# Optimization experiments

Hardware: AMD Instinct MI355X
Metric: run time of the kernel (lower is better)

The kernel has to match this reference:

```python
import jax, jax.numpy as jnp
import numpy as np

B, P = 65536, 22  # sets, max players per freeze frame
IN, HID, OUT = 6, 64, 128


def setup_inputs() -> dict:
    key = jax.random.key(0)
    k0, k1, k2, k3, k4, k5 = jax.random.split(key, 6)
    pitch = jnp.array([120.0, 80.0], dtype=jnp.float32)
    player_locs = jax.random.uniform(k0, (B, P, 2), dtype=jnp.float32) * pitch
    actor_locs = jax.random.uniform(k1, (B, 2), dtype=jnp.float32) * pitch
    # teammate / keeper flags in {0,1}
    flags = jax.random.randint(k2, (B, P, 2), 0, 2).astype(jnp.float32)
    # validity mask: 0 -> player skipped (simulates ragged / missing entries)
    mask = jax.random.randint(k3, (B, P), 0, 2).astype(jnp.int32)
    W1 = jax.random.normal(k4, (IN, HID), dtype=jnp.float32) / np.sqrt(IN)
    b1 = jnp.zeros((HID,), dtype=jnp.float32)
    W2 = jax.random.normal(k5, (HID, OUT), dtype=jnp.float32) / np.sqrt(HID)
    b2 = jnp.zeros((OUT,), dtype=jnp.float32)
    return {"player_locs": player_locs, "actor_locs": actor_locs, "flags": flags,
            "mask": mask, "W1": W1, "b1": b1, "W2": W2, "b2": b2}


def reference(player_locs, actor_locs, flags, mask, W1, b1, W2, b2):
    # per-player features relative to the actor: [dx, dy, dist, angle, teammate, keeper]
    dxy = player_locs - actor_locs[:, None, :]                 # [B,P,2]
    dist = jnp.sqrt(jnp.sum(dxy * dxy, axis=-1, keepdims=True))  # [B,P,1]
    angle = jnp.arctan2(dxy[..., 1:2], dxy[..., 0:1])            # [B,P,1]
    feats = jnp.concatenate([dxy, dist, angle, flags], axis=-1)  # [B,P,6]
    # PlayerMLP: Linear -> ReLU -> Linear
    h = jax.nn.relu(jnp.einsum('bpi,ih->bph', feats, W1) + b1)   # [B,P,64]
    emb = jnp.einsum('bph,ho->bpo', h, W2) + b2                  # [B,P,128]
    # masked mean over valid players; empty sets yield zeros (sum is 0)
    m = mask.astype(emb.dtype)[..., None]                        # [B,P,1]
    cnt = jnp.sum(m, axis=1)                                     # [B,1]
    pooled = jnp.sum(emb * m, axis=1) / jnp.maximum(cnt, 1.0)    # [B,128]
    return pooled
```

## Files before the change

### kernel.cpp

```cpp
#include <hip/hip_runtime.h>
#include <math.h>

#define PMAX 22
#define HID 64
#define OUTD 128
#define SETS_PER_WAVE 8
#define WAVES_PER_BLOCK 4

typedef __attribute__((ext_vector_type(8))) short short8;
typedef __attribute__((ext_vector_type(4))) float float4v;

__device__ __forceinline__ float rl(float v, int l) {
    return __int_as_float(__builtin_amdgcn_readlane(__float_as_int(v), l));
}
__device__ __forceinline__ unsigned bf16_bits(float x) {
    unsigned u = __float_as_uint(x);
    return (u + 0x7FFFu + ((u >> 16) & 1u)) >> 16;
}
__device__ __forceinline__ void wave_lds_sync() {
    asm volatile("s_waitcnt lgkmcnt(0)" ::: "memory");
    __builtin_amdgcn_wave_barrier();
}

__global__ __launch_bounds__(256) void set_encoder_kernel(
    const float* __restrict__ player_locs,
    const float* __restrict__ actor_locs,
    const float* __restrict__ flags,
    const int*   __restrict__ mask,
    const float* __restrict__ W1,
    const float* __restrict__ b1,
    const float* __restrict__ W2,
    const float* __restrict__ b2,
    float* __restrict__ out)
{
    __shared__ __align__(16) unsigned w2f[16 * 256];
    __shared__ __align__(16) unsigned short hb[WAVES_PER_BLOCK][SETS_PER_WAVE][HID + 4];

    const int tid  = threadIdx.x;
    const int lane = tid & 63;
    const int wave = tid >> 6;

    const int wave_id = blockIdx.x * WAVES_PER_BLOCK + wave;
    const int set0    = wave_id * SETS_PER_WAVE;

    {
        const int pr = tid >> 3;
        const int nt = tid & 7;
        const float* rA = W2 + (size_t)(2 * pr) * OUTD + 16 * nt;
        const float* rB = rA + OUTD;
        float ra[16], rb[16];
#pragma unroll
        for (int i = 0; i < 4; ++i) {
            *(float4*)&ra[4 * i] = ((const float4*)rA)[i];
            *(float4*)&rb[4 * i] = ((const float4*)rB)[i];
        }
        const int kt = pr >> 4;
        const int kk = (2 * pr) & 31;
        const int Q  = kk >> 3;
        const int j2 = (kk >> 1) & 3;
        const int base = ((kt * 8 + nt) * 4 + Q) * 64 + j2;
#pragma unroll
        for (int c = 0; c < 16; ++c)
            w2f[base + 4 * c] = bf16_bits(ra[c]) | (bf16_bits(rb[c]) << 16);
    }

    const float w10 = W1[0 * HID + lane];
    const float w11 = W1[1 * HID + lane];
    const float w12 = W1[2 * HID + lane];
    const float w13 = W1[3 * HID + lane];
    const float w14 = W1[4 * HID + lane];
    const float w15 = W1[5 * HID + lane];
    const float b1l = b1[lane];

    __syncthreads();

    float fr[4][6];
    unsigned long long bm[4];
#pragma unroll
    for (int g = 0; g < 4; ++g) {
        const int lidx = lane < 2 * PMAX ? lane : 2 * PMAX - 1;
        const int grow = (set0 + 2 * g) * PMAX + lidx;
        float2 pl = ((const float2*)player_locs)[grow];
        float2 fl = ((const float2*)flags)[grow];
        int    m  = mask[grow];
        const int sl = 2 * g + (lidx >= PMAX ? 1 : 0);
        float2 ac = ((const float2*)actor_locs)[set0 + sl];
        float dx = pl.x - ac.x;
        float dy = pl.y - ac.y;
        fr[g][0] = dx;
        fr[g][1] = dy;
        fr[g][2] = sqrtf(dx * dx + dy * dy);
        fr[g][3] = atan2f(dy, dx);
        fr[g][4] = fl.x;
        fr[g][5] = fl.y;
        bm[g] = __ballot((lane < 2 * PMAX) && (m != 0));
    }

    float hs[SETS_PER_WAVE];
    unsigned nonempty = 0;
#pragma unroll
    for (int s = 0; s < SETS_PER_WAVE; ++s) {
        const int g    = s >> 1;
        const int base = (s & 1) * PMAX;
        unsigned bits = (unsigned)(bm[g] >> base) & 0x3FFFFFu;
        const int cnt = __builtin_popcount(bits);
        if (bits) nonempty |= (1u << s);
        float acc = 0.0f;
        unsigned bb = bits;
        while (bb) {
            const int p = __builtin_ctz(bb);
            bb &= bb - 1;
            const int src = base + p;
            float f0 = rl(fr[g][0], src);
            float f1 = rl(fr[g][1], src);
            float f2 = rl(fr[g][2], src);
            float f3 = rl(fr[g][3], src);
            float f4 = rl(fr[g][4], src);
            float f5 = rl(fr[g][5], src);
            float t0 = fmaf(f0, w10, b1l);
            t0 = fmaf(f1, w11, t0);
            t0 = fmaf(f2, w12, t0);
            float t1 = f3 * w13;
            t1 = fmaf(f4, w14, t1);
            t1 = fmaf(f5, w15, t1);
            acc += fmaxf(t0 + t1, 0.0f);
        }
        hs[s] = acc * (1.0f / fmaxf((float)cnt, 1.0f));
    }

#pragma unroll
    for (int s = 0; s < SETS_PER_WAVE; ++s)
        hb[wave][s][lane] = (unsigned short)bf16_bits(hs[s]);
    wave_lds_sync();

    const int Q  = lane >> 4;
    const int sA = lane & 7;
    short8 afrag[2];
#pragma unroll
    for (int kt = 0; kt < 2; ++kt) {
        uint2 p0 = *(const uint2*)&hb[wave][sA][32 * kt + 8 * Q];
        uint2 p1 = *(const uint2*)&hb[wave][sA][32 * kt + 8 * Q + 4];
        union { unsigned u[4]; short8 s8; } cv;
        cv.u[0] = p0.x; cv.u[1] = p0.y; cv.u[2] = p1.x; cv.u[3] = p1.y;
        afrag[kt] = cv.s8;
    }

    float4v acc[8];
#pragma unroll
    for (int nt = 0; nt < 8; ++nt) {
        union { uint4 u4; short8 s8; } f0, f1;
        f0.u4 = *(const uint4*)&w2f[(0 * 8 + nt) * 256 + 4 * lane];
        f1.u4 = *(const uint4*)&w2f[(1 * 8 + nt) * 256 + 4 * lane];
        float4v z = {0.0f, 0.0f, 0.0f, 0.0f};
        acc[nt] = __builtin_amdgcn_mfma_f32_16x16x32_bf16(afrag[0], f0.s8, z, 0, 0, 0);
        acc[nt] = __builtin_amdgcn_mfma_f32_16x16x32_bf16(afrag[1], f1.s8, acc[nt], 0, 0, 0);
    }

    const int c = lane & 15;
    float b2v[8];
#pragma unroll
    for (int nt = 0; nt < 8; ++nt) b2v[nt] = b2[16 * nt + c];

    if (Q < 2) {
        const unsigned nsh = nonempty >> (4 * Q);
#pragma unroll
        for (int nt = 0; nt < 8; ++nt) {
#pragma unroll
            for (int r = 0; r < 4; ++r) {
                const int s = 4 * Q + r;
                const float f = (float)((nsh >> r) & 1u);
                out[(size_t)(set0 + s) * OUTD + 16 * nt + c] = acc[nt][r] + f * b2v[nt];
            }
        }
    }
}

extern "C" void kernel_launch(void* const* d_in, const int* in_sizes, int n_in,
                              void* d_out, int out_size, void* d_ws, size_t ws_size,
                              hipStream_t stream) {
    const float* player_locs = (const float*)d_in[0];
    const float* actor_locs  = (const float*)d_in[1];
    const float* flags       = (const float*)d_in[2];
    const int*   mask        = (const int*)d_in[3];
    const float* W1          = (const float*)d_in[4];
    const float* b1          = (const float*)d_in[5];
    const float* W2          = (const float*)d_in[6];
    const float* b2          = (const float*)d_in[7];
    float*       out         = (float*)d_out;

    const int B = in_sizes[0] / (PMAX * 2);
    const int sets_per_block = WAVES_PER_BLOCK * SETS_PER_WAVE;
    const int grid = (B + sets_per_block - 1) / sets_per_block;

    hipLaunchKernelGGL(set_encoder_kernel, dim3(grid), dim3(256), 0, stream,
                       player_locs, actor_locs, flags, mask, W1, b1, W2, b2, out);
}
```

Measured before the change: 122.3 us.

## Pack player features to fp16 pairs and use fdot2 with fast atan2

Packs the six per-player features and W1 columns into fp16 pairs, halving the readlane broadcasts and replacing six FMAs with three dot2 instructions in the serial per-player loop. It also replaces atan2f with a polynomial approximation and sqrtf with the hardware sqrt. This trades feature precision (fp16 for distances up to about 144) for fewer scalar broadcasts and fewer VALU instructions.

```diff
diff --git a/kernel.cpp b/kernel.cpp
--- a/kernel.cpp
+++ b/kernel.cpp
@@ -9,9 +9,26 @@
 
 typedef __attribute__((ext_vector_type(8))) short short8;
 typedef __attribute__((ext_vector_type(4))) float float4v;
-
-__device__ __forceinline__ float rl(float v, int l) {
-    return __int_as_float(__builtin_amdgcn_readlane(__float_as_int(v), l));
+typedef _Float16 fh2 __attribute__((ext_vector_type(2)));
+
+__device__ __forceinline__ int rl_i(int v, int l) {
+    return __builtin_amdgcn_readlane(v, l);
+}
+__device__ __forceinline__ int pk2(float x, float y) {
+    auto v = __builtin_amdgcn_cvt_pkrtz(x, y);
+    union { decltype(v) h; int i; } c;
+    c.h = v;
+    return c.i;
+}
+__device__ __forceinline__ float fdot2i(int a, int b, float c) {
+    union { int i; fh2 h; } ua, ub;
+    ua.i = a;
+    ub.i = b;
+#if defined(__has_builtin) && __has_builtin(__builtin_amdgcn_fdot2)
+    return __builtin_amdgcn_fdot2(ua.h, ub.h, c, false);
+#else
+    return fmaf((float)ua.h.x, (float)ub.h.x, fmaf((float)ua.h.y, (float)ub.h.y, c));
+#endif
 }
 __device__ __forceinline__ unsigned bf16_bits(float x) {
     unsigned u = __float_as_uint(x);
@@ -20,6 +37,16 @@
 __device__ __forceinline__ void wave_lds_sync() {
     asm volatile("s_waitcnt lgkmcnt(0)" ::: "memory");
     __builtin_amdgcn_wave_barrier();
+}
+__device__ __forceinline__ float fast_atan2(float y, float x) {
+    float ax = fabsf(x), ay = fabsf(y);
+    float mn = fminf(ax, ay), mx = fmaxf(ax, ay);
+    float a = mn * __builtin_amdgcn_rcpf(fmaxf(mx, 1e-30f));
+    float s = a * a;
+    float r = a * fmaf(s, fmaf(s, fmaf(s, -0.0851330f, 0.1801410f), -0.3302995f), 0.9998660f);
+    if (ay > ax) r = 1.57079637f - r;
+    if (x < 0.0f) r = 3.14159274f - r;
+    return copysignf(r, y);
 }
 
 __global__ __launch_bounds__(256) void set_encoder_kernel(
@@ -64,17 +91,14 @@
             w2f[base + 4 * c] = bf16_bits(ra[c]) | (bf16_bits(rb[c]) << 16);
     }
 
-    const float w10 = W1[0 * HID + lane];
-    const float w11 = W1[1 * HID + lane];
-    const float w12 = W1[2 * HID + lane];
-    const float w13 = W1[3 * HID + lane];
-    const float w14 = W1[4 * HID + lane];
-    const float w15 = W1[5 * HID + lane];
+    const int w01 = pk2(W1[0 * HID + lane], W1[1 * HID + lane]);
+    const int w23 = pk2(W1[2 * HID + lane], W1[3 * HID + lane]);
+    const int w45 = pk2(W1[4 * HID + lane], W1[5 * HID + lane]);
     const float b1l = b1[lane];
 
     __syncthreads();
 
-    float fr[4][6];
+    int fh[4][3];
     unsigned long long bm[4];
 #pragma unroll
     for (int g = 0; g < 4; ++g) {
@@ -87,12 +111,11 @@
         float2 ac = ((const float2*)actor_locs)[set0 + sl];
         float dx = pl.x - ac.x;
         float dy = pl.y - ac.y;
-        fr[g][0] = dx;
-        fr[g][1] = dy;
-        fr[g][2] = sqrtf(dx * dx + dy * dy);
-        fr[g][3] = atan2f(dy, dx);
-        fr[g][4] = fl.x;
-        fr[g][5] = fl.y;
+        float dist = __builtin_amdgcn_sqrtf(fmaf(dx, dx, dy * dy));
+        float ang  = fast_atan2(dy, dx);
+        fh[g][0] = pk2(dx, dy);
+        fh[g][1] = pk2(dist, ang);
+        fh[g][2] = pk2(fl.x, fl.y);
         bm[g] = __ballot((lane < 2 * PMAX) && (m != 0));
     }
 
@@ -111,19 +134,13 @@
             const int p = __builtin_ctz(bb);
             bb &= bb - 1;
             const int src = base + p;
-            float f0 = rl(fr[g][0], src);
-            float f1 = rl(fr[g][1], src);
-            float f2 = rl(fr[g][2], src);
-            float f3 = rl(fr[g][3], src);
-            float f4 = rl(fr[g][4], src);
-            float f5 = rl(fr[g][5], src);
-            float t0 = fmaf(f0, w10, b1l);
-            t0 = fmaf(f1, w11, t0);
-            t0 = fmaf(f2, w12, t0);
-            float t1 = f3 * w13;
-            t1 = fmaf(f4, w14, t1);
-            t1 = fmaf(f5, w15, t1);
-            acc += fmaxf(t0 + t1, 0.0f);
+            const int u0 = rl_i(fh[g][0], src);
+            const int u1 = rl_i(fh[g][1], src);
+            const int u2 = rl_i(fh[g][2], src);
+            float t = fdot2i(u0, w01, b1l);
+            t = fdot2i(u1, w23, t);
+            t = fdot2i(u2, w45, t);
+            acc += fmaxf(t, 0.0f);
         }
         hs[s] = acc * (1.0f / fmaxf((float)cnt, 1.0f));
     }
```

After: 112.6 us. -8.0%, faster.
